# Performance work log

Measured on AMD Instinct MI355X. Metric: run time of the kernel, lower is better.

The kernel has to match this reference:

```python
import jax, jax.numpy as jnp
import numpy as np

N_HEAD = 8


def _norm(x):
    # torch: (x - x.mean()) / x.std()  -- global, unbiased std (ddof=1)
    return (x - x.mean()) / x.std(ddof=1)


def _floyd_block2(x, w_qkv, scale):
    # x: [b, n, n, c]; w_qkv: [5c, c] (torch Linear weight layout)
    x = _norm(x)
    b, n, _, c = x.shape
    qkv = x @ w_qkv.T  # [b, n, n, 5c]
    q, k1, k2, v1, v2 = jnp.split(qkv, 5, axis=-1)

    def heads(t):  # 'b i j (h d) -> b h i j d'
        return t.reshape(b, n, n, N_HEAD, c // N_HEAD).transpose(0, 3, 1, 2, 4)

    q, k1, k2, v1, v2 = map(heads, (q, k1, k2, v1, v2))
    # pivotal attention: for pair (i,j) attend over pivot p with two k/v branches
    s = (jnp.einsum('bhijd,bhipd->bhijp', q, k1)
         + jnp.einsum('bhijd,bhpjd->bhijp', q, k2)) * scale  # [b,h,i,j,p]
    a = jax.nn.softmax(s, axis=-1)
    o = (jnp.einsum('bhijp,bhipd->bhijd', a, v1)
         + jnp.einsum('bhijp,bhpjd->bhijd', a, v2))
    # 'b h i j d -> b i j (h d)'
    return o.transpose(0, 2, 3, 1, 4).reshape(b, n, n, c)


def setup_inputs() -> dict:
    key = jax.random.key(0)
    k1, k2, k3, k4 = jax.random.split(key, 4)
    b, n, c, depth = 4, 96, 256, 4
    adj = jax.random.randint(k1, (b, n, n), 0, 2, dtype=jnp.int64)
    emb_w = jax.random.normal(k2, (128, c), dtype=jnp.float32)  # std 1.0 per init_weights
    qkv_w = jax.random.normal(k3, (depth, 5 * c, c), dtype=jnp.float32) * (c ** -0.5)
    head_w = jax.random.normal(k4, (c, c), dtype=jnp.float32) * 0.02
    head_b = jnp.zeros((c,), dtype=jnp.float32)
    return {'adj': adj, 'emb_w': emb_w, 'qkv_w': qkv_w,
            'head_w': head_w, 'head_b': head_b}


def reference(adj, emb_w, qkv_w, head_w, head_b):
    c = emb_w.shape[1]
    head_dim = c // N_HEAD
    scale = head_dim ** (-0.5) * 50.0  # FloydBlock2 scale
    x = emb_w[adj]  # [b, n, n, c]
    for l in range(qkv_w.shape[0]):
        x = _floyd_block2(x, qkv_w[l], scale)
    x = x.mean(axis=(1, 2))           # mean over (i, j) -> [b, c]
    x = jax.lax.stop_gradient(x)      # blocks run under torch.no_grad
    return x @ head_w.T + head_b
```

## Files before the change

### kernel.cpp

```cpp
#include <hip/hip_runtime.h>

#define B_ 4
#define N_ 96
#define C_ 256
#define NPAIR (B_*N_*N_)
#define CE (NPAIR*C_)
#define SCALE 8.838834764831844f

typedef __attribute__((ext_vector_type(4))) float f32x4;
typedef __attribute__((ext_vector_type(8))) __bf16 bf16x8;
typedef __attribute__((ext_vector_type(4))) __bf16 bf16x4;
typedef __attribute__((ext_vector_type(4))) unsigned short u16x4;
typedef __attribute__((ext_vector_type(8))) unsigned short u16x8;

__device__ __forceinline__ unsigned short f2bf(float f){
  __bf16 h = (__bf16)f;
  return __builtin_bit_cast(unsigned short, h);
}
__device__ __forceinline__ float bf2f(unsigned short u){
  union { unsigned int i; float f; } v; v.i = ((unsigned int)u) << 16; return v.f;
}
__device__ __forceinline__ f32x4 vmax4(f32x4 a, f32x4 b){
  f32x4 r; r.x=fmaxf(a.x,b.x); r.y=fmaxf(a.y,b.y); r.z=fmaxf(a.z,b.z); r.w=fmaxf(a.w,b.w); return r;
}

__device__ __forceinline__ void gload16(const void* g, void* l){
  __builtin_amdgcn_global_load_lds((const __attribute__((address_space(1))) unsigned int*)g,
                                   (__attribute__((address_space(3))) unsigned int*)l,
                                   16, 0, 0);
}

__global__ __launch_bounds__(256) void k_init(float* __restrict__ z){
  for (int i = threadIdx.x; i < 1536; i += 256) z[i] = 0.f;
}

__global__ __launch_bounds__(256) void k_gather(const int* __restrict__ adj,
                                                const float* __restrict__ emb,
                                                unsigned short* __restrict__ xb,
                                                float2* __restrict__ part){
  int tid = threadIdx.x;
  int lp = tid >> 4, lane16 = tid & 15;
  int pair = blockIdx.x*16 + lp;
  int row = adj[pair];
  const f32x4* src = (const f32x4*)(emb + (size_t)row*C_);
  u16x4*       dst = (u16x4*)(xb + (size_t)pair*C_);
  float s = 0.f, q = 0.f;
  for (int v = 0; v < 4; ++v){
    f32x4 t = src[v*16 + lane16];
    u16x4 o;
    o.x = f2bf(t.x); o.y = f2bf(t.y); o.z = f2bf(t.z); o.w = f2bf(t.w);
    dst[v*16 + lane16] = o;
    s += t.x + t.y + t.z + t.w;
    q += t.x*t.x + t.y*t.y + t.z*t.z + t.w*t.w;
  }
  __shared__ float rs[256], rq[256];
  rs[tid] = s; rq[tid] = q; __syncthreads();
  for (int o = 128; o > 0; o >>= 1){
    if (tid < o){ rs[tid] += rs[tid+o]; rq[tid] += rq[tid+o]; }
    __syncthreads();
  }
  if (tid == 0){
    float* pp = (float*)&part[blockIdx.x & 63];
    atomicAdd(pp, rs[0]); atomicAdd(pp+1, rq[0]);
  }
}

__global__ __launch_bounds__(256) void k_wconv(const float* __restrict__ w,
                                               unsigned short* __restrict__ wb,
                                               float* __restrict__ wsum){
  int row  = blockIdx.x*4 + (threadIdx.x >> 6);
  int lane = threadIdx.x & 63;
  f32x4 v = ((const f32x4*)(w + (size_t)row*256))[lane];
  u16x4 o;
  o.x = f2bf(v.x); o.y = f2bf(v.y); o.z = f2bf(v.z); o.w = f2bf(v.w);
  ((u16x4*)(wb + (size_t)row*256))[lane] = o;
  float s = v.x + v.y + v.z + v.w;
  for (int m = 32; m > 0; m >>= 1) s += __shfl_down(s, m);
  if (lane == 0) wsum[row] = s;
}

__global__ __launch_bounds__(256) void k_gemm(const unsigned short* __restrict__ Xb,
                                              const unsigned short* __restrict__ W,
                                              const float* __restrict__ wsum_l,
                                              const float2* __restrict__ part,
                                              unsigned short* __restrict__ qkv5){
  __shared__ unsigned short smem[128*128];
  unsigned short* As = smem;
  unsigned short* Bs = smem + 128*64;
  const int tid = threadIdx.x;
  const int w = tid >> 6, lane = tid & 63;
  const int quad = lane >> 4, l16 = lane & 15;
  const int m0 = blockIdx.y * 128, n0 = blockIdx.x * 128;
  const int mw = (w & 1) * 64, nw = (w >> 1) * 64;
  double S = 0.0, Q = 0.0;
  for (int i = 0; i < 64; ++i){ float2 pp = part[i]; S += (double)pp.x; Q += (double)pp.y; }
  const float mean = (float)(S / (double)CE);
  const float rstd = (float)(1.0 / sqrt((Q - S*S/(double)CE) / (double)(CE - 1)));
  f32x4 acc[4][4] = {};

  for (int kt = 0; kt < 256; kt += 64){
    const int rbase = w * 32;
    const int rowoff = lane >> 3;
    const int kg = (lane & 7) ^ rowoff;
    for (int i8 = 0; i8 < 4; ++i8){
      int row = rbase + i8*8 + rowoff;
      gload16(Xb + (size_t)(m0+row)*256 + kt + kg*8, &As[(rbase + i8*8)*64]);
      gload16(W  + (size_t)(n0+row)*256 + kt + kg*8, &Bs[(rbase + i8*8)*64]);
    }
    __syncthreads();
    for (int ks = 0; ks < 2; ++ks){
      bf16x8 af[4], bf[4];
      for (int t4 = 0; t4 < 4; ++t4){
        int rm = mw + t4*16 + l16;
        af[t4] = *(const bf16x8*)((const char*)As + rm*128 + ((((ks<<2)|quad) ^ (rm&7))*16));
        int rn = nw + t4*16 + l16;
        bf[t4] = *(const bf16x8*)((const char*)Bs + rn*128 + ((((ks<<2)|quad) ^ (rn&7))*16));
      }
      for (int mi = 0; mi < 4; ++mi)
        for (int ni = 0; ni < 4; ++ni)
          acc[mi][ni] = __builtin_amdgcn_mfma_f32_16x16x32_bf16(af[mi], bf[ni], acc[mi][ni], 0, 0, 0);
    }
    __syncthreads();
  }

  float ws[4];
  #pragma unroll
  for (int ni = 0; ni < 4; ++ni) ws[ni] = wsum_l[n0 + nw + ni*16 + l16];
  for (int mi = 0; mi < 4; ++mi)
    for (int ni = 0; ni < 4; ++ni)
      for (int r = 0; r < 4; ++r){
        int row = mw + mi*16 + quad*4 + r;
        int col = nw + ni*16 + l16;
        float val = rstd*(acc[mi][ni][r] - mean*ws[ni]);
        smem[row*128 + col] = f2bf(val);
      }
  __syncthreads();

  const int t_slab = n0 >> 8;
  const int hbase  = (n0 >> 5) & 7;
  unsigned short* slab = qkv5 + (size_t)t_slab*CE;
  const int trow = tid >> 4;
  const int tcol = (tid & 15) * 8;
  const int h  = hbase + (tcol >> 5);
  const int dd = tcol & 31;
  for (int pass = 0; pass < 8; ++pass){
    int row = pass*16 + trow;
    int gm = m0 + row;
    int b = gm / 9216; int rem = gm - b*9216;
    int ii = rem / 96, jj = rem - (rem/96)*96;
    u16x8 vv = *(const u16x8*)&smem[row*128 + tcol];
    *(u16x8*)&slab[(((size_t)(b*8+h)*96 + ii)*96 + jj)*32 + dd] = vv;
  }
}

__global__ __launch_bounds__(256) void k_scores1(const unsigned short* __restrict__ qkv5,
                                                 unsigned short* __restrict__ s1){
  __shared__ unsigned short Qs[96*40], Ks[96*40];
  __shared__ unsigned short Ss[96*100];
  int wg = blockIdx.x; int bh = wg/96, ic = wg - bh*96;
  int tid = threadIdx.x;
  size_t gslab = (size_t)wg*3072;
  const unsigned short* qp = qkv5 + 0*(size_t)CE + gslab;
  const unsigned short* kp = qkv5 + 1*(size_t)CE + gslab;
  for (int g = tid; g < 768; g += 256){
    int j = g >> 3, q4 = g & 7;
    *(u16x4*)&Qs[j*40 + q4*4] = *(const u16x4*)&qp[j*32 + q4*4];
    *(u16x4*)&Ks[j*40 + q4*4] = *(const u16x4*)&kp[j*32 + q4*4];
  }
  __syncthreads();
  int w = tid >> 6, lane = tid & 63, quad = lane >> 4, l16 = lane & 15;
  #pragma unroll
  for (int r = 0; r < 9; ++r){
    int tile = w*9 + r; int jt = tile/6, pt = tile - jt*6;
    bf16x8 a = *(const bf16x8*)((const char*)Qs + (jt*16 + l16)*80 + quad*16);
    bf16x8 b = *(const bf16x8*)((const char*)Ks + (pt*16 + l16)*80 + quad*16);
    f32x4 c = {0.f,0.f,0.f,0.f};
    c = __builtin_amdgcn_mfma_f32_16x16x32_bf16(a, b, c, 0, 0, 0);
    int col = pt*16 + l16;
    #pragma unroll
    for (int rr = 0; rr < 4; ++rr){
      int row = jt*16 + quad*4 + rr;
      _Float16 hv = (_Float16)(c[rr] * SCALE);
      Ss[row*100 + col] = __builtin_bit_cast(unsigned short, hv);
    }
  }
  __syncthreads();
  for (int g = tid; g < 1152; g += 256){
    int j = g / 12, c8 = g - j*12;
    *(u16x8*)&s1[((size_t)(bh*96 + j))*9216 + ic*96 + c8*8] = *(const u16x8*)&Ss[j*100 + c8*8];
  }
}

__global__ __launch_bounds__(256) void k_attn2(const unsigned short* __restrict__ qkv5,
                                               const unsigned short* __restrict__ s1,
                                               unsigned short* __restrict__ a_out,
                                               unsigned short* __restrict__ xb){
  __shared__ unsigned short Qs[96*40], Ks[96*40], Vd[32*100];
  __shared__ unsigned short SsPb[96*104];
  __shared__ float Mx[192], Sx[192];
  int wg = blockIdx.x; int bh = wg/96, jj = wg - bh*96;
  int b = bh >> 3, h = bh & 7;
  int tid = threadIdx.x;
  int w = tid >> 6, lane = tid & 63, quad = lane >> 4, l16 = lane & 15;
  const unsigned short* qn  = qkv5 + 0*(size_t)CE;
  const unsigned short* k2n = qkv5 + 2*(size_t)CE;
  const unsigned short* v2n = qkv5 + 4*(size_t)CE;
  if (tid < 192){ Mx[tid] = -1e30f; Sx[tid] = 0.f; }
  const unsigned short* s1g = s1 + ((size_t)bh*96 + jj)*9216;
  for (int k = w; k < 18; k += 4)
    gload16(s1g + k*512 + lane*8, &SsPb[k*512]);
  for (int g = tid; g < 768; g += 256){
    int r7 = g & 7, q4 = (g >> 3) & 7, a8 = g >> 6;
    int p = r7 + a8*8;
    size_t base = (((size_t)bh*96 + p)*96 + jj)*32 + q4*4;
    *(u16x4*)&Qs[p*40 + q4*4] = *(const u16x4*)&qn[base];
    *(u16x4*)&Ks[p*40 + q4*4] = *(const u16x4*)&k2n[base];
    u16x4 v = *(const u16x4*)&v2n[base];
    int d0 = q4*4;
    Vd[(d0+0)*100 + p] = v.x; Vd[(d0+1)*100 + p] = v.y;
    Vd[(d0+2)*100 + p] = v.z; Vd[(d0+3)*100 + p] = v.w;
  }
  __syncthreads();
  f32x4 sc[9];
  #pragma unroll
  for (int r = 0; r < 9; ++r){
    int tile = w*9 + r; int it = tile/6, pt = tile - it*6;
    bf16x8 a = *(const bf16x8*)((const char*)Qs + (it*16 + l16)*80 + quad*16);
    bf16x8 bb = *(const bf16x8*)((const char*)Ks + (pt*16 + l16)*80 + quad*16);
    f32x4 c = {0.f,0.f,0.f,0.f};
    c = __builtin_amdgcn_mfma_f32_16x16x32_bf16(a, bb, c, 0, 0, 0);
    int col = pt*16 + l16;
    #pragma unroll
    for (int rr = 0; rr < 4; ++rr){
      int row = it*16 + quad*4 + rr;
      _Float16 hv = __builtin_bit_cast(_Float16, SsPb[row*96 + col]);
      sc[r][rr] = c[rr]*SCALE + (float)hv;
    }
  }
  const bool odd = (w & 1);
  const int itA = (w*9)/6, itB = itA + 1;
  const int slot = w & 1;
  f32x4 vA = {-1e30f,-1e30f,-1e30f,-1e30f}, vB = vA;
  #pragma unroll
  for (int r = 0; r < 9; ++r){
    bool inA = odd ? (r < 3) : (r < 6);
    if (inA) vA = vmax4(vA, sc[r]); else vB = vmax4(vB, sc[r]);
  }
  #pragma unroll
  for (int m = 1; m < 16; m <<= 1){
    f32x4 t;
    t.x=__shfl_xor(vA.x,m); t.y=__shfl_xor(vA.y,m); t.z=__shfl_xor(vA.z,m); t.w=__shfl_xor(vA.w,m);
    vA = vmax4(vA, t);
    t.x=__shfl_xor(vB.x,m); t.y=__shfl_xor(vB.y,m); t.z=__shfl_xor(vB.z,m); t.w=__shfl_xor(vB.w,m);
    vB = vmax4(vB, t);
  }
  if (l16 < 4){
    float va = (l16==0)?vA.x:(l16==1)?vA.y:(l16==2)?vA.z:vA.w;
    float vb = (l16==0)?vB.x:(l16==1)?vB.y:(l16==2)?vB.z:vB.w;
    Mx[(itA*16 + quad*4 + l16)*2 + slot] = va;
    Mx[(itB*16 + quad*4 + l16)*2 + slot] = vb;
  }
  __syncthreads();
  f32x4 mA, mB;
  #pragma unroll
  for (int rr = 0; rr < 4; ++rr){
    float2 ta = *(const float2*)&Mx[(itA*16 + quad*4 + rr)*2];
    float2 tb = *(const float2*)&Mx[(itB*16 + quad*4 + rr)*2];
    mA[rr] = fmaxf(ta.x, ta.y); mB[rr] = fmaxf(tb.x, tb.y);
  }
  f32x4 sA = {0.f,0.f,0.f,0.f}, sB = {0.f,0.f,0.f,0.f};
  #pragma unroll
  for (int r = 0; r < 9; ++r){
    bool inA = odd ? (r < 3) : (r < 6);
    #pragma unroll
    for (int rr = 0; rr < 4; ++rr){
      float m = inA ? mA[rr] : mB[rr];
      float e = __expf(sc[r][rr] - m);
      sc[r][rr] = e;
      if (inA) sA[rr] += e; else sB[rr] += e;
    }
  }
  #pragma unroll
  for (int m = 1; m < 16; m <<= 1){
    f32x4 t;
    t.x=__shfl_xor(sA.x,m); t.y=__shfl_xor(sA.y,m); t.z=__shfl_xor(sA.z,m); t.w=__shfl_xor(sA.w,m);
    sA += t;
    t.x=__shfl_xor(sB.x,m); t.y=__shfl_xor(sB.y,m); t.z=__shfl_xor(sB.z,m); t.w=__shfl_xor(sB.w,m);
    sB += t;
  }
  if (l16 < 4){
    float va = (l16==0)?sA.x:(l16==1)?sA.y:(l16==2)?sA.z:sA.w;
    float vb = (l16==0)?sB.x:(l16==1)?sB.y:(l16==2)?sB.z:sB.w;
    Sx[(itA*16 + quad*4 + l16)*2 + slot] = va;
    Sx[(itB*16 + quad*4 + l16)*2 + slot] = vb;
  }
  __syncthreads();
  f32x4 iA, iB;
  #pragma unroll
  for (int rr = 0; rr < 4; ++rr){
    float2 ta = *(const float2*)&Sx[(itA*16 + quad*4 + rr)*2];
    float2 tb = *(const float2*)&Sx[(itB*16 + quad*4 + rr)*2];
    iA[rr] = 1.f/(ta.x + ta.y); iB[rr] = 1.f/(tb.x + tb.y);
  }
  #pragma unroll
  for (int r = 0; r < 9; ++r){
    int tile = w*9 + r; int it = tile/6, pt = tile - it*6;
    int col = pt*16 + l16;
    bool inA = odd ? (r < 3) : (r < 6);
    #pragma unroll
    for (int rr = 0; rr < 4; ++rr){
      int row = it*16 + quad*4 + rr;
      float inv = inA ? iA[rr] : iB[rr];
      SsPb[row*104 + col] = f2bf(sc[r][rr] * inv);
    }
  }
  __syncthreads();
  unsigned short* ap = a_out + (size_t)bh*96*9216 + (size_t)jj*96;
  for (int g = tid; g < 1152; g += 256){
    int i = g / 12, c = g - i*12;
    *(u16x8*)&ap[(size_t)i*9216 + c*8] = *(const u16x8*)&SsPb[i*104 + c*8];
  }
  #pragma unroll
  for (int r = 0; r < 3; ++r){
    int tile = w*3 + r; int it = tile >> 1, dt = tile & 1;
    f32x4 c = {0.f,0.f,0.f,0.f};
    #pragma unroll
    for (int kp3 = 0; kp3 < 3; ++kp3){
      bf16x8 a = *(const bf16x8*)((const char*)SsPb + (it*16 + l16)*208 + kp3*64 + quad*16);
      const char* vb = (const char*)Vd + (dt*16 + l16)*200 + kp3*64 + quad*16;
      bf16x4 lo = *(const bf16x4*)vb;
      bf16x4 hi = *(const bf16x4*)(vb + 8);
      bf16x8 bb = __builtin_shufflevector(lo, hi, 0,1,2,3,4,5,6,7);
      c = __builtin_amdgcn_mfma_f32_16x16x32_bf16(a, bb, c, 0, 0, 0);
    }
    int d = dt*16 + l16;
    #pragma unroll
    for (int rr = 0; rr < 4; ++rr){
      int i = it*16 + quad*4 + rr;
      xb[(((size_t)b*96 + i)*96 + jj)*256 + h*32 + d] = f2bf(c[rr]);
    }
  }
}

__global__ __launch_bounds__(256) void k_attn1(const unsigned short* __restrict__ a_in,
                                               const unsigned short* __restrict__ qkv5,
                                               unsigned short* __restrict__ xb,
                                               float2* __restrict__ statsPart,
                                               float* __restrict__ poolAcc,
                                               int last){
  __shared__ unsigned short As[96*104], Vd[32*100];
  __shared__ float redS[256], redQ[256];
  __shared__ float poolL[32];
  int wg = blockIdx.x; int bh = wg/96, ii = wg - bh*96;
  int b = bh >> 3, h = bh & 7;
  int tid = threadIdx.x;
  if (tid < 32) poolL[tid] = 0.f;
  const unsigned short* vp = qkv5 + 3*(size_t)CE + ((size_t)bh*96 + ii)*3072;
  for (int g = tid; g < 768; g += 256){
    int r7 = g & 7, q4 = (g >> 3) & 7, a8 = g >> 6;
    int p = r7 + a8*8;
    u16x4 v = *(const u16x4*)&vp[p*32 + q4*4];
    int d0 = q4*4;
    Vd[(d0+0)*100 + p] = v.x; Vd[(d0+1)*100 + p] = v.y;
    Vd[(d0+2)*100 + p] = v.z; Vd[(d0+3)*100 + p] = v.w;
  }
  const unsigned short* ain = a_in + ((size_t)bh*96 + ii)*9216;
  for (int g = tid; g < 1152; g += 256){
    int j = g / 12, c = g - j*12;
    *(u16x8*)&As[j*104 + c*8] = *(const u16x8*)&ain[j*96 + c*8];
  }
  __syncthreads();
  int w = tid >> 6, lane = tid & 63, quad = lane >> 4, l16 = lane & 15;
  float ls = 0.f, lq = 0.f;
  #pragma unroll
  for (int r = 0; r < 3; ++r){
    int tile = w*3 + r; int jt = tile >> 1, dt = tile & 1;
    f32x4 c = {0.f,0.f,0.f,0.f};
    #pragma unroll
    for (int kp3 = 0; kp3 < 3; ++kp3){
      bf16x8 a = *(const bf16x8*)((const char*)As + (jt*16 + l16)*208 + kp3*64 + quad*16);
      const char* vb = (const char*)Vd + (dt*16 + l16)*200 + kp3*64 + quad*16;
      bf16x4 lo = *(const bf16x4*)vb;
      bf16x4 hi = *(const bf16x4*)(vb + 8);
      bf16x8 bb = __builtin_shufflevector(lo, hi, 0,1,2,3,4,5,6,7);
      c = __builtin_amdgcn_mfma_f32_16x16x32_bf16(a, bb, c, 0, 0, 0);
    }
    int d = dt*16 + l16;
    float dsum = 0.f;
    #pragma unroll
    for (int rr = 0; rr < 4; ++rr){
      int j = jt*16 + quad*4 + rr;
      size_t xi = (((size_t)b*96 + ii)*96 + j)*256 + h*32 + d;
      float val = bf2f(xb[xi]) + c[rr];
      if (!last){ xb[xi] = f2bf(val); ls += val; lq += val*val; }
      else dsum += val;
    }
    if (last) atomicAdd(&poolL[d], dsum);
  }
  if (!last){
    redS[tid] = ls; redQ[tid] = lq; __syncthreads();
    for (int o = 128; o > 0; o >>= 1){
      if (tid < o){ redS[tid] += redS[tid+o]; redQ[tid] += redQ[tid+o]; }
      __syncthreads();
    }
    if (tid == 0){
      float* pp = (float*)&statsPart[blockIdx.x & 63];
      atomicAdd(pp, redS[0]); atomicAdd(pp+1, redQ[0]);
    }
  } else {
    __syncthreads();
    if (tid < 32) atomicAdd(&poolAcc[b*256 + h*32 + tid], poolL[tid]);
  }
}

__global__ __launch_bounds__(256) void k_head(const float* __restrict__ poolAcc,
                                              const float* __restrict__ hw,
                                              const float* __restrict__ hb,
                                              float* __restrict__ out){
  int b = blockIdx.x, t = threadIdx.x;
  __shared__ float xm[256];
  xm[t] = poolAcc[b*256 + t] * (1.0f/9216.0f);
  __syncthreads();
  float o = hb[t];
  for (int c = 0; c < 256; ++c) o += xm[c] * hw[t*256 + c];
  out[b*256 + t] = o;
}

extern "C" void kernel_launch(void* const* d_in, const int* in_sizes, int n_in,
                              void* d_out, int out_size, void* d_ws, size_t ws_size,
                              hipStream_t stream){
  (void)in_sizes; (void)n_in; (void)out_size; (void)ws_size;
  const int*   adj  = (const int*)d_in[0];
  const float* emb  = (const float*)d_in[1];
  const float* qkvw = (const float*)d_in[2];
  const float* hw   = (const float*)d_in[3];
  const float* hb   = (const float*)d_in[4];

  char* p = (char*)d_ws;
  unsigned short* xb   = (unsigned short*)p; p += (size_t)CE*2;
  unsigned short* qkv5 = (unsigned short*)p; p += (size_t)5*CE*2;
  unsigned short* s1   = (unsigned short*)p; p += (size_t)32*96*9216*2;
  unsigned short* aP   = (unsigned short*)p; p += (size_t)32*96*9216*2;
  unsigned short* wbf  = (unsigned short*)p; p += (size_t)4*1280*256*2;
  float*          wsum = (float*)p;          p += (size_t)4*1280*4;
  float2*         part = (float2*)p;         p += 4*64*sizeof(float2);
  float*          pool = (float*)p;          p += 1024*sizeof(float);

  k_init  <<<dim3(1),     dim3(256), 0, stream>>>((float*)part);
  k_gather<<<dim3(2304),  dim3(256), 0, stream>>>(adj, emb, xb, part);
  k_wconv <<<dim3(1280),  dim3(256), 0, stream>>>(qkvw, wbf, wsum);
  for (int l = 0; l < 4; ++l){
    k_gemm   <<<dim3(10, 288), dim3(256), 0, stream>>>(xb, wbf + (size_t)l*1280*256,
                                                       wsum + l*1280, part + l*64, qkv5);
    k_scores1<<<dim3(3072),    dim3(256), 0, stream>>>(qkv5, s1);
    k_attn2  <<<dim3(3072),    dim3(256), 0, stream>>>(qkv5, s1, aP, xb);
    k_attn1  <<<dim3(3072),    dim3(256), 0, stream>>>(aP, qkv5, xb,
                                                       part + (l+1 < 4 ? (l+1)*64 : 0),
                                                       pool, (l == 3) ? 1 : 0);
  }
  k_head<<<dim3(4), dim3(256), 0, stream>>>(pool, hw, hb, (float*)d_out);
}
```

Baseline: 694.8 us.

## Remap GEMM blocks per XCD, pad epilogue smem, pool last layer directly

The QKV GEMM now uses a 1D grid whose block index is remapped so that consecutive M tiles land on the same XCD, which should improve L2 reuse of the X rows across the 10 N tiles. The epilogue staging buffer gets a padded row stride (132) to reduce LDS bank conflicts. On the last layer, attn2 no longer writes its output to xb and attn1 no longer reads xb back. Each kernel instead accumulates its own contribution straight into the pooled sum, which removes a full activation write and read. In exchange there are more shared and global atomics in the final layer.

```diff
diff --git a/kernel.cpp b/kernel.cpp
--- a/kernel.cpp
+++ b/kernel.cpp
@@ -6,6 +6,7 @@
 #define NPAIR (B_*N_*N_)
 #define CE (NPAIR*C_)
 #define SCALE 8.838834764831844f
+#define CP 132
 
 typedef __attribute__((ext_vector_type(4))) float f32x4;
 typedef __attribute__((ext_vector_type(8))) __bf16 bf16x8;
@@ -84,13 +85,16 @@
                                               const float* __restrict__ wsum_l,
                                               const float2* __restrict__ part,
                                               unsigned short* __restrict__ qkv5){
-  __shared__ unsigned short smem[128*128];
+  __shared__ unsigned short smem[128*CP];
   unsigned short* As = smem;
   unsigned short* Bs = smem + 128*64;
   const int tid = threadIdx.x;
   const int w = tid >> 6, lane = tid & 63;
   const int quad = lane >> 4, l16 = lane & 15;
-  const int m0 = blockIdx.y * 128, n0 = blockIdx.x * 128;
+  const int L = blockIdx.x;
+  const int xcd = L & 7, rest = L >> 3;
+  const int nt = rest % 10, kt2 = rest / 10;
+  const int m0 = (xcd + 8*kt2) * 128, n0 = nt * 128;
   const int mw = (w & 1) * 64, nw = (w >> 1) * 64;
   double S = 0.0, Q = 0.0;
   for (int i = 0; i < 64; ++i){ float2 pp = part[i]; S += (double)pp.x; Q += (double)pp.y; }
@@ -132,7 +136,7 @@
         int row = mw + mi*16 + quad*4 + r;
         int col = nw + ni*16 + l16;
         float val = rstd*(acc[mi][ni][r] - mean*ws[ni]);
-        smem[row*128 + col] = f2bf(val);
+        smem[row*CP + col] = f2bf(val);
       }
   __syncthreads();
 
@@ -148,7 +152,7 @@
     int gm = m0 + row;
     int b = gm / 9216; int rem = gm - b*9216;
     int ii = rem / 96, jj = rem - (rem/96)*96;
-    u16x8 vv = *(const u16x8*)&smem[row*128 + tcol];
+    u16x8 vv = *(const u16x8*)&smem[row*CP + tcol];
     *(u16x8*)&slab[(((size_t)(b*8+h)*96 + ii)*96 + jj)*32 + dd] = vv;
   }
 }
@@ -194,10 +198,13 @@
 __global__ __launch_bounds__(256) void k_attn2(const unsigned short* __restrict__ qkv5,
                                                const unsigned short* __restrict__ s1,
                                                unsigned short* __restrict__ a_out,
-                                               unsigned short* __restrict__ xb){
+                                               unsigned short* __restrict__ xb,
+                                               float* __restrict__ poolAcc,
+                                               int last){
   __shared__ unsigned short Qs[96*40], Ks[96*40], Vd[32*100];
   __shared__ unsigned short SsPb[96*104];
   __shared__ float Mx[192], Sx[192];
+  __shared__ float poolL[32];
   int wg = blockIdx.x; int bh = wg/96, jj = wg - bh*96;
   int b = bh >> 3, h = bh & 7;
   int tid = threadIdx.x;
@@ -206,6 +213,7 @@
   const unsigned short* k2n = qkv5 + 2*(size_t)CE;
   const unsigned short* v2n = qkv5 + 4*(size_t)CE;
   if (tid < 192){ Mx[tid] = -1e30f; Sx[tid] = 0.f; }
+  if (tid < 32) poolL[tid] = 0.f;
   const unsigned short* s1g = s1 + ((size_t)bh*96 + jj)*9216;
   for (int k = w; k < 18; k += 4)
     gload16(s1g + k*512 + lane*8, &SsPb[k*512]);
@@ -334,11 +342,19 @@
       c = __builtin_amdgcn_mfma_f32_16x16x32_bf16(a, bb, c, 0, 0, 0);
     }
     int d = dt*16 + l16;
-    #pragma unroll
-    for (int rr = 0; rr < 4; ++rr){
-      int i = it*16 + quad*4 + rr;
-      xb[(((size_t)b*96 + i)*96 + jj)*256 + h*32 + d] = f2bf(c[rr]);
-    }
+    if (!last){
+      #pragma unroll
+      for (int rr = 0; rr < 4; ++rr){
+        int i = it*16 + quad*4 + rr;
+        xb[(((size_t)b*96 + i)*96 + jj)*256 + h*32 + d] = f2bf(c[rr]);
+      }
+    } else {
+      atomicAdd(&poolL[d], c[0] + c[1] + c[2] + c[3]);
+    }
+  }
+  if (last){
+    __syncthreads();
+    if (tid < 32) atomicAdd(&poolAcc[b*256 + h*32 + tid], poolL[tid]);
   }
 }
 
@@ -386,16 +402,17 @@
       c = __builtin_amdgcn_mfma_f32_16x16x32_bf16(a, bb, c, 0, 0, 0);
     }
     int d = dt*16 + l16;
-    float dsum = 0.f;
-    #pragma unroll
-    for (int rr = 0; rr < 4; ++rr){
-      int j = jt*16 + quad*4 + rr;
-      size_t xi = (((size_t)b*96 + ii)*96 + j)*256 + h*32 + d;
-      float val = bf2f(xb[xi]) + c[rr];
-      if (!last){ xb[xi] = f2bf(val); ls += val; lq += val*val; }
-      else dsum += val;
-    }
-    if (last) atomicAdd(&poolL[d], dsum);
+    if (!last){
+      #pragma unroll
+      for (int rr = 0; rr < 4; ++rr){
+        int j = jt*16 + quad*4 + rr;
+        size_t xi = (((size_t)b*96 + ii)*96 + j)*256 + h*32 + d;
+        float val = bf2f(xb[xi]) + c[rr];
+        xb[xi] = f2bf(val); ls += val; lq += val*val;
+      }
+    } else {
+      atomicAdd(&poolL[d], c[0] + c[1] + c[2] + c[3]);
+    }
   }
   if (!last){
     redS[tid] = ls; redQ[tid] = lq; __syncthreads();
@@ -450,13 +467,14 @@
   k_gather<<<dim3(2304),  dim3(256), 0, stream>>>(adj, emb, xb, part);
   k_wconv <<<dim3(1280),  dim3(256), 0, stream>>>(qkvw, wbf, wsum);
   for (int l = 0; l < 4; ++l){
-    k_gemm   <<<dim3(10, 288), dim3(256), 0, stream>>>(xb, wbf + (size_t)l*1280*256,
+    int last = (l == 3) ? 1 : 0;
+    k_gemm   <<<dim3(2880),    dim3(256), 0, stream>>>(xb, wbf + (size_t)l*1280*256,
                                                        wsum + l*1280, part + l*64, qkv5);
     k_scores1<<<dim3(3072),    dim3(256), 0, stream>>>(qkv5, s1);
-    k_attn2  <<<dim3(3072),    dim3(256), 0, stream>>>(qkv5, s1, aP, xb);
+    k_attn2  <<<dim3(3072),    dim3(256), 0, stream>>>(qkv5, s1, aP, xb, pool, last);
     k_attn1  <<<dim3(3072),    dim3(256), 0, stream>>>(aP, qkv5, xb,
                                                        part + (l+1 < 4 ? (l+1)*64 : 0),
-                                                       pool, (l == 3) ? 1 : 0);
+                                                       pool, last);
   }
   k_head<<<dim3(4), dim3(256), 0, stream>>>(pool, hw, hb, (float*)d_out);
 }
```

New measurement: 649.9 us. -6.5%, faster.
